# Kernel optimization log

Measured on AMD Instinct MI355X. Metric: run time of the kernel, lower is better.

## Reference

```python
import jax, jax.numpy as jnp
import numpy as np

N_QUBITS = 10
QLCU_LAYERS = 2
GATE_LAYERS = 2
FEATURE_DIM = 256
OUTPUT_DIM = 1
BATCH = 2048
TWO_PI = float(2.0 * np.pi)
N_MEAS = 3 * N_QUBITS


def _ang(theta, B):
    # broadcast scalar or (B,) angle to (B,) float32
    return jnp.broadcast_to(jnp.asarray(theta, jnp.float32), (B,))


def _apply_1q(psi, U, wire):
    # psi: (B,)+(2,)*n ; U: (B,2,2) complex64
    pm = jnp.moveaxis(psi, wire + 1, -1)
    out = jnp.einsum('bij,b...j->b...i', U, pm)
    return jnp.moveaxis(out, -1, wire + 1)


def rx(psi, theta, wire):
    B = psi.shape[0]
    t = _ang(theta, B) * 0.5
    c = jnp.cos(t).astype(jnp.complex64)
    s = (-1j) * jnp.sin(t).astype(jnp.complex64)
    U = jnp.stack([jnp.stack([c, s], -1), jnp.stack([s, c], -1)], -2)
    return _apply_1q(psi, U, wire)


def ry(psi, theta, wire):
    B = psi.shape[0]
    t = _ang(theta, B) * 0.5
    c = jnp.cos(t).astype(jnp.complex64)
    s = jnp.sin(t).astype(jnp.complex64)
    U = jnp.stack([jnp.stack([c, -s], -1), jnp.stack([s, c], -1)], -2)
    return _apply_1q(psi, U, wire)


def rz(psi, theta, wire):
    # diagonal: e^{-i t/2}, e^{+i t/2}
    B = psi.shape[0]
    n = psi.ndim - 1
    t = _ang(theta, B) * 0.5
    ph = jnp.exp(1j * jnp.stack([-t, t], -1).astype(jnp.complex64))  # (B,2)
    pm = jnp.moveaxis(psi, wire + 1, -1)
    pm = pm * ph.reshape((B,) + (1,) * (n - 1) + (2,))
    return jnp.moveaxis(pm, -1, wire + 1)


def _mv2(psi, a, b):
    return jnp.moveaxis(psi, (a + 1, b + 1), (-2, -1))


def _mv2_back(pm, a, b):
    return jnp.moveaxis(pm, (-2, -1), (a + 1, b + 1))


def crz(psi, theta, control, target):
    # diagonal on (control,target): [1, 1, e^{-it/2}, e^{+it/2}]
    B = psi.shape[0]
    n = psi.ndim - 1
    t = (_ang(theta, B) * 0.5).astype(jnp.complex64)
    e_m = jnp.exp(-1j * t)
    e_p = jnp.exp(1j * t)
    one = jnp.ones_like(e_m)
    P = jnp.stack([jnp.stack([one, one], -1), jnp.stack([e_m, e_p], -1)], -2)  # (B,2,2)
    pm = _mv2(psi, control, target)
    pm = pm * P.reshape((B,) + (1,) * (n - 2) + (2, 2))
    return _mv2_back(pm, control, target)


def ising_xx(psi, theta, a, b):
    # exp(-i t/2 XX): cos(t/2) I - i sin(t/2) X(x)X (bit-flip both)
    B = psi.shape[0]
    n = psi.ndim - 1
    t = _ang(theta, B) * 0.5
    c = jnp.cos(t).astype(jnp.complex64).reshape((B,) + (1,) * n)
    s = jnp.sin(t).astype(jnp.complex64).reshape((B,) + (1,) * n)
    pm = _mv2(psi, a, b)
    out = c * pm - 1j * s * pm[..., ::-1, ::-1]
    return _mv2_back(out, a, b)


def ising_yy(psi, theta, a, b):
    # exp(-i t/2 YY): (YY psi)[ta,tb] = (-1 if ta==tb else +1) * psi[flip]
    B = psi.shape[0]
    n = psi.ndim - 1
    t = _ang(theta, B) * 0.5
    c = jnp.cos(t).astype(jnp.complex64).reshape((B,) + (1,) * n)
    s = jnp.sin(t).astype(jnp.complex64).reshape((B,) + (1,) * n)
    sign = jnp.array([[-1.0, 1.0], [1.0, -1.0]], jnp.complex64)
    pm = _mv2(psi, a, b)
    out = c * pm - 1j * s * sign * pm[..., ::-1, ::-1]
    return _mv2_back(out, a, b)


def measure_xyz(psi):
    # expvals [X0..X_{n-1}, Y0.., Z0..] -> (B, 3n) float32
    n = psi.ndim - 1
    xs, ys, zs = [], [], []
    for w in range(n):
        pm = jnp.moveaxis(psi, w + 1, -1)
        p0, p1 = pm[..., 0], pm[..., 1]
        axes = tuple(range(1, n))
        a = jnp.sum(jnp.conj(p0) * p1, axis=axes)
        xs.append(2.0 * jnp.real(a))
        ys.append(2.0 * jnp.imag(a))
        zs.append(jnp.sum(jnp.abs(p0) ** 2 - jnp.abs(p1) ** 2, axis=axes))
    return jnp.stack(xs + ys + zs, axis=1).astype(jnp.float32)


def selective_ssm(psi, qlcu, bpar, cpar, dtpar, n, layers):
    idx = 0
    for _ in range(layers):
        for i in range(n):
            psi = ry(psi, qlcu[:, idx], i); idx += 1
        for i in range(n):
            psi = ising_xx(psi, qlcu[:, idx], i, (i + 1) % n); idx += 1
        for i in range(n):
            psi = ry(psi, bpar[i], i)
        for i in range(n):
            psi = ry(psi, qlcu[:, idx], i); idx += 1
        for i in range(n):
            psi = ising_yy(psi, qlcu[:, idx], i, (i + 1) % n); idx += 1
        for i in range(n):
            psi = rz(psi, cpar[i], i)
        for i in range(n):
            psi = rx(psi, dtpar[i], i)
    return psi


def gating(psi, gp, n, layers):
    idx = 0
    for _ in range(layers):
        for i in range(n):
            psi = rx(psi, gp[idx], i); idx += 1
        for i in range(n - 1):
            psi = crz(psi, gp[idx], i, i + 1); idx += 1
        for i in range(n):
            psi = ry(psi, gp[idx], i); idx += 1
        if n > 1:
            psi = crz(psi, gp[idx], n - 1, 0); idx += 1
    return psi


def skip_circuit(psi, sp, n):
    idx = 0
    for i in range(n):
        psi = rx(psi, sp[idx], i); idx += 1
    for i in range(n):
        psi = ry(psi, sp[idx], i); idx += 1
    for i in range(n):
        psi = rz(psi, sp[idx], i); idx += 1
    return psi


def _forward(x, W_proj, b_proj, qlcu_base, gate_base, skip_base, b_params, c_params, dt_params,
             W1, b1, W2, b2, W3, b3, w1, w2, w3, W_out, b_out):
    B = x.shape[0]
    n = N_QUBITS
    proj = x @ W_proj.T + b_proj
    qlcu = jax.nn.sigmoid(proj) * TWO_PI + qlcu_base[None, :]
    psi0 = jnp.zeros((B, 2 ** n), jnp.complex64).at[:, 0].set(1.0).reshape((B,) + (2,) * n)
    m1 = measure_xyz(selective_ssm(psi0, qlcu, b_params, c_params, dt_params, n, QLCU_LAYERS))
    # branches 2/3 have batch-independent params and initial state -> compute once, broadcast
    psi1 = jnp.zeros((1, 2 ** n), jnp.complex64).at[:, 0].set(1.0).reshape((1,) + (2,) * n)
    m2 = jnp.broadcast_to(measure_xyz(gating(psi1, gate_base, n, GATE_LAYERS)), (B, N_MEAS))
    m3 = jnp.broadcast_to(measure_xyz(skip_circuit(psi1, skip_base, n)), (B, N_MEAS))
    y1 = m1 @ W1.T + b1
    y2 = m2 @ W2.T + b2
    y3 = m3 @ W3.T + b3
    comb = w1 * y1 + w2 * y2 + w3 * y3
    return comb @ W_out.T + b_out


def setup_inputs() -> dict:
    key = jax.random.key(0)
    ks = jax.random.split(key, 17)
    nq = N_QUBITS
    n_qlcu = 4 * nq * QLCU_LAYERS
    n_gate = 4 * nq * GATE_LAYERS
    n_skip = 3 * nq
    lim_p = 1.0 / np.sqrt(FEATURE_DIM)
    lim_m = 1.0 / np.sqrt(N_MEAS)
    return dict(
        x=jax.random.normal(ks[0], (BATCH, FEATURE_DIM), jnp.float32),
        W_proj=jax.random.uniform(ks[1], (n_qlcu, FEATURE_DIM), jnp.float32, -lim_p, lim_p),
        b_proj=jax.random.uniform(ks[2], (n_qlcu,), jnp.float32, -lim_p, lim_p),
        qlcu_base=jax.random.uniform(ks[3], (n_qlcu,), jnp.float32, 0.0, TWO_PI),
        gate_base=jax.random.uniform(ks[4], (n_gate,), jnp.float32, 0.0, TWO_PI),
        skip_base=jax.random.uniform(ks[5], (n_skip,), jnp.float32, 0.0, TWO_PI),
        b_params=jax.random.uniform(ks[6], (nq,), jnp.float32, 0.0, TWO_PI),
        c_params=jax.random.uniform(ks[7], (nq,), jnp.float32, 0.0, TWO_PI),
        dt_params=jax.random.uniform(ks[8], (nq,), jnp.float32, 0.0, TWO_PI),
        W1=jax.random.uniform(ks[9], (N_MEAS, N_MEAS), jnp.float32, -lim_m, lim_m),
        b1=jax.random.uniform(ks[10], (N_MEAS,), jnp.float32, -lim_m, lim_m),
        W2=jax.random.uniform(ks[11], (N_MEAS, N_MEAS), jnp.float32, -lim_m, lim_m),
        b2=jax.random.uniform(ks[12], (N_MEAS,), jnp.float32, -lim_m, lim_m),
        W3=jax.random.uniform(ks[13], (N_MEAS, N_MEAS), jnp.float32, -lim_m, lim_m),
        b3=jax.random.uniform(ks[14], (N_MEAS,), jnp.float32, -lim_m, lim_m),
        w1=jnp.ones((1,), jnp.float32),
        w2=jnp.ones((1,), jnp.float32),
        w3=jnp.ones((1,), jnp.float32),
        W_out=jax.random.uniform(ks[15], (OUTPUT_DIM, N_MEAS), jnp.float32, -lim_m, lim_m),
        b_out=jax.random.uniform(ks[16], (OUTPUT_DIM,), jnp.float32, -lim_m, lim_m),
    )


def reference(x, W_proj, b_proj, qlcu_base, gate_base, skip_base, b_params, c_params, dt_params,
              W1, b1, W2, b2, W3, b3, w1, w2, w3, W_out, b_out):
    return _forward(x, W_proj, b_proj, qlcu_base, gate_base, skip_base, b_params, c_params, dt_params,
                    W1, b1, W2, b2, W3, b3, w1, w2, w3, W_out, b_out)
```

## Files before the change

### kernel.cpp

```cpp
#include <hip/hip_runtime.h>
#include <math.h>

#define TPB 320
#define TWO_PI_F 6.283185307179586f


#define ALLQ(OP) OP(0) OP(1) OP(2) OP(3) OP(4) OP(5) OP(6) OP(7) OP(8) OP(9)
#define ALLQ9(OP) OP(0) OP(1) OP(2) OP(3) OP(4) OP(5) OP(6) OP(7) OP(8)

template<int CTRL>
__device__ __forceinline__ float dppmv(float v) {
    return __builtin_bit_cast(float,
        __builtin_amdgcn_update_dpp(0, __builtin_bit_cast(int, v), CTRL, 0xF, 0xF, true));
}

template<int LM>
__device__ __forceinline__ float lx(float v, int lane) {
    (void)lane;
    if constexpr (LM == 1)       return dppmv<0xB1>(v);
    else if constexpr (LM == 2)  return dppmv<0x4E>(v);
    else if constexpr (LM == 3)  return dppmv<0x1B>(v);
    else if constexpr (LM == 4)  return dppmv<0x1B>(dppmv<0x141>(v));
    else if constexpr (LM == 6)  return dppmv<0xB1>(dppmv<0x141>(v));
    else if constexpr (LM == 8)  return dppmv<0x128>(v);
    else if constexpr (LM == 12) return dppmv<0x1B>(dppmv<0x140>(v));
    else                         return __shfl_xor(v, LM);
}


template<int W>
__device__ __forceinline__ void g_ry(float (&re)[16], float (&im)[16], float c, float s, int lane) {
    if constexpr (W <= 5) {
        constexpr int LM = 1 << (5 - W);
        const float ss = ((lane >> (5 - W)) & 1) ? s : -s;
        float pr[16], pi[16];
#pragma unroll
        for (int r = 0; r < 16; ++r) { pr[r] = lx<LM>(re[r], lane); pi[r] = lx<LM>(im[r], lane); }
#pragma unroll
        for (int r = 0; r < 16; ++r) {
            re[r] = fmaf(ss, pr[r], c * re[r]);
            im[r] = fmaf(ss, pi[r], c * im[r]);
        }
    } else {
        constexpr int MK = 1 << (9 - W);
#pragma unroll
        for (int r = 0; r < 16; ++r) {
            if ((r & MK) == 0) {
                const int r1 = r | MK;
                float r0 = re[r], i0 = im[r], r1v = re[r1], i1 = im[r1];
                re[r]  = fmaf(-s, r1v, c * r0);
                im[r]  = fmaf(-s, i1,  c * i0);
                re[r1] = fmaf( s, r0,  c * r1v);
                im[r1] = fmaf( s, i0,  c * i1);
            }
        }
    }
}

template<int W>
__device__ __forceinline__ void g_rx(float (&re)[16], float (&im)[16], float c, float s, int lane) {
    if constexpr (W <= 5) {
        constexpr int LM = 1 << (5 - W);
        float pr[16], pi[16];
#pragma unroll
        for (int r = 0; r < 16; ++r) { pr[r] = lx<LM>(re[r], lane); pi[r] = lx<LM>(im[r], lane); }
#pragma unroll
        for (int r = 0; r < 16; ++r) {
            re[r] = fmaf( s, pi[r], c * re[r]);
            im[r] = fmaf(-s, pr[r], c * im[r]);
        }
    } else {
        constexpr int MK = 1 << (9 - W);
#pragma unroll
        for (int r = 0; r < 16; ++r) {
            if ((r & MK) == 0) {
                const int r1 = r | MK;
                float r0 = re[r], i0 = im[r], r1v = re[r1], i1 = im[r1];
                re[r]  = fmaf( s, i1,  c * r0);
                im[r]  = fmaf(-s, r1v, c * i0);
                re[r1] = fmaf( s, i0,  c * r1v);
                im[r1] = fmaf(-s, r0,  c * i1);
            }
        }
    }
}

template<int W>
__device__ __forceinline__ void g_rz(float (&re)[16], float (&im)[16], float c, float s, int lane) {
    if constexpr (W <= 5) {
        const float sp = ((lane >> (5 - W)) & 1) ? s : -s;
#pragma unroll
        for (int r = 0; r < 16; ++r) {
            float rr = re[r], ii = im[r];
            re[r] = rr * c - ii * sp;
            im[r] = ii * c + rr * sp;
        }
    } else {
        constexpr int MK = 1 << (9 - W);
#pragma unroll
        for (int r = 0; r < 16; ++r) {
            const float sp = (r & MK) ? s : -s;
            float rr = re[r], ii = im[r];
            re[r] = rr * c - ii * sp;
            im[r] = ii * c + rr * sp;
        }
    }
}

template<int C, int T>
__device__ __forceinline__ void g_crz(float (&re)[16], float (&im)[16], float c, float s, int lane) {
#pragma unroll
    for (int r = 0; r < 16; ++r) {
        const int cb = (C <= 5) ? ((lane >> (5 - C)) & 1) : ((r >> (9 - C)) & 1);
        const int tb = (T <= 5) ? ((lane >> (5 - T)) & 1) : ((r >> (9 - T)) & 1);
        const float cc  = cb ? c : 1.f;
        const float sp2 = cb ? (tb ? s : -s) : 0.f;
        float rr = re[r], ii = im[r];
        re[r] = cc * rr - sp2 * ii;
        im[r] = cc * ii + sp2 * rr;
    }
}

template<int A, int Bq, bool YY>
__device__ __forceinline__ void g_xy(float (&re)[16], float (&im)[16], float c, float s, int lane) {
    constexpr int bpA = 9 - A, bpB = 9 - Bq;
    constexpr int LM   = ((bpA >= 4) ? (1 << (bpA - 4)) : 0) | ((bpB >= 4) ? (1 << (bpB - 4)) : 0);
    constexpr int LOCM = ((bpA < 4) ? (1 << bpA) : 0) | ((bpB < 4) ? (1 << bpB) : 0);
    float pr[16], pi[16];
#pragma unroll
    for (int r = 0; r < 16; ++r) {
        float vr = re[r ^ LOCM], vi = im[r ^ LOCM];
        if constexpr (LM != 0) { pr[r] = lx<LM>(vr, lane); pi[r] = lx<LM>(vi, lane); }
        else                   { pr[r] = vr; pi[r] = vi; }
    }
#pragma unroll
    for (int r = 0; r < 16; ++r) {
        float sg;
        if constexpr (YY) {
            const int bA = (A  <= 5) ? ((lane >> (5 - A )) & 1) : ((r >> (9 - A )) & 1);
            const int bB = (Bq <= 5) ? ((lane >> (5 - Bq)) & 1) : ((r >> (9 - Bq)) & 1);
            sg = (bA == bB) ? -s : s;
        } else sg = s;
        float rr = re[r], ii = im[r];
        re[r] = fmaf( sg, pi[r], c * rr);
        im[r] = fmaf(-sg, pr[r], c * ii);
    }
}

template<int W>
__device__ __forceinline__ void g_u1(float (&re)[16], float (&im)[16], const float* U, int lane) {
    const float u00r=U[0], u00i=U[1], u01r=U[2], u01i=U[3];
    const float u10r=U[4], u10i=U[5], u11r=U[6], u11i=U[7];
    if constexpr (W <= 5) {
        constexpr int LM = 1 << (5 - W);
        const int side = (lane >> (5 - W)) & 1;
        const float aR = side ? u11r : u00r, aI = side ? u11i : u00i;
        const float bR = side ? u10r : u01r, bI = side ? u10i : u01i;
        float pr[16], pi[16];
#pragma unroll
        for (int r = 0; r < 16; ++r) { pr[r] = lx<LM>(re[r], lane); pi[r] = lx<LM>(im[r], lane); }
#pragma unroll
        for (int r = 0; r < 16; ++r) {
            float rr = re[r], ii = im[r];
            float nr = aR * rr; nr = fmaf(-aI, ii, nr); nr = fmaf(bR, pr[r], nr); nr = fmaf(-bI, pi[r], nr);
            float ni = aR * ii; ni = fmaf( aI, rr, ni); ni = fmaf(bR, pi[r], ni); ni = fmaf( bI, pr[r], ni);
            re[r] = nr; im[r] = ni;
        }
    } else {
        constexpr int MK = 1 << (9 - W);
#pragma unroll
        for (int r = 0; r < 16; ++r) {
            if ((r & MK) == 0) {
                const int r1 = r | MK;
                float r0 = re[r], i0 = im[r], r1v = re[r1], i1 = im[r1];
                float a = u00r*r0; a = fmaf(-u00i, i0, a); a = fmaf(u01r, r1v, a); a = fmaf(-u01i, i1, a);
                float b = u00r*i0; b = fmaf( u00i, r0, b); b = fmaf(u01r, i1,  b); b = fmaf( u01i, r1v, b);
                float c = u10r*r0; c = fmaf(-u10i, i0, c); c = fmaf(u11r, r1v, c); c = fmaf(-u11i, i1, c);
                float d = u10r*i0; d = fmaf( u10i, r0, d); d = fmaf(u11r, i1,  d); d = fmaf( u11i, r1v, d);
                re[r] = a; im[r] = b; re[r1] = c; im[r1] = d;
            }
        }
    }
}


__device__ __forceinline__ void g_ry2_01(float (&re)[16], float (&im)[16],
                                         float c0, float s0, float c1, float s1, int lane) {
    float ar[16], ai[16], br[16], bi[16], cr2[16], ci2[16];
#pragma unroll
    for (int r = 0; r < 16; ++r) { ar[r] = lx<32>(re[r], lane); ai[r] = lx<32>(im[r], lane); }
#pragma unroll
    for (int r = 0; r < 16; ++r) { br[r] = lx<16>(re[r], lane); bi[r] = lx<16>(im[r], lane); }
#pragma unroll
    for (int r = 0; r < 16; ++r) { cr2[r] = lx<48>(re[r], lane); ci2[r] = lx<48>(im[r], lane); }
    const float sg0 = ((lane >> 5) & 1) ? s0 : -s0;
    const float sg1 = ((lane >> 4) & 1) ? s1 : -s1;
    const float k0 = c0 * c1, k1 = c1 * sg0, k2 = c0 * sg1, k3 = sg0 * sg1;
#pragma unroll
    for (int r = 0; r < 16; ++r) {
        float o_r = k0 * re[r];
        o_r = fmaf(k1, ar[r], o_r); o_r = fmaf(k2, br[r], o_r); o_r = fmaf(k3, cr2[r], o_r);
        float o_i = k0 * im[r];
        o_i = fmaf(k1, ai[r], o_i); o_i = fmaf(k2, bi[r], o_i); o_i = fmaf(k3, ci2[r], o_i);
        re[r] = o_r; im[r] = o_i;
    }
}

__device__ __forceinline__ void g_rx2_01(float (&re)[16], float (&im)[16],
                                         float c0, float s0, float c1, float s1, int lane) {
    float ar[16], ai[16], br[16], bi[16], cr2[16], ci2[16];
#pragma unroll
    for (int r = 0; r < 16; ++r) { ar[r] = lx<32>(re[r], lane); ai[r] = lx<32>(im[r], lane); }
#pragma unroll
    for (int r = 0; r < 16; ++r) { br[r] = lx<16>(re[r], lane); bi[r] = lx<16>(im[r], lane); }
#pragma unroll
    for (int r = 0; r < 16; ++r) { cr2[r] = lx<48>(re[r], lane); ci2[r] = lx<48>(im[r], lane); }
    const float k0 = c0 * c1, kA = c1 * s0, kB = c0 * s1, kC = s0 * s1;
#pragma unroll
    for (int r = 0; r < 16; ++r) {
        float rr = re[r], ii = im[r];
        float o_r = k0 * rr;
        o_r = fmaf(kA, ai[r], o_r); o_r = fmaf(kB, bi[r], o_r); o_r = fmaf(-kC, cr2[r], o_r);
        float o_i = k0 * ii;
        o_i = fmaf(-kA, ar[r], o_i); o_i = fmaf(-kB, br[r], o_i); o_i = fmaf(-kC, ci2[r], o_i);
        re[r] = o_r; im[r] = o_i;
    }
}

__device__ __forceinline__ void g_u2_01(float (&re)[16], float (&im)[16],
                                        const float* U0, const float* U1, int lane) {
    const int b0 = (lane >> 5) & 1, b1 = (lane >> 4) & 1;
    const float u0o_r = U0[(b0*2+b0)*2],       u0o_i = U0[(b0*2+b0)*2+1];
    const float u0f_r = U0[(b0*2+(b0^1))*2],   u0f_i = U0[(b0*2+(b0^1))*2+1];
    const float u1o_r = U1[(b1*2+b1)*2],       u1o_i = U1[(b1*2+b1)*2+1];
    const float u1f_r = U1[(b1*2+(b1^1))*2],   u1f_i = U1[(b1*2+(b1^1))*2+1];
    const float K00r = u0o_r*u1o_r - u0o_i*u1o_i, K00i = u0o_r*u1o_i + u0o_i*u1o_r;
    const float K01r = u0o_r*u1f_r - u0o_i*u1f_i, K01i = u0o_r*u1f_i + u0o_i*u1f_r;
    const float K10r = u0f_r*u1o_r - u0f_i*u1o_i, K10i = u0f_r*u1o_i + u0f_i*u1o_r;
    const float K11r = u0f_r*u1f_r - u0f_i*u1f_i, K11i = u0f_r*u1f_i + u0f_i*u1f_r;
    float ar[16], ai[16], br[16], bi[16], cr2[16], ci2[16];
#pragma unroll
    for (int r = 0; r < 16; ++r) { ar[r] = lx<32>(re[r], lane); ai[r] = lx<32>(im[r], lane); }
#pragma unroll
    for (int r = 0; r < 16; ++r) { br[r] = lx<16>(re[r], lane); bi[r] = lx<16>(im[r], lane); }
#pragma unroll
    for (int r = 0; r < 16; ++r) { cr2[r] = lx<48>(re[r], lane); ci2[r] = lx<48>(im[r], lane); }
#pragma unroll
    for (int r = 0; r < 16; ++r) {
        float rr = re[r], ii = im[r];
        float o_r = K00r * rr;         o_r = fmaf(-K00i, ii, o_r);
        o_r = fmaf(K01r, br[r], o_r);  o_r = fmaf(-K01i, bi[r], o_r);
        o_r = fmaf(K10r, ar[r], o_r);  o_r = fmaf(-K10i, ai[r], o_r);
        o_r = fmaf(K11r, cr2[r], o_r); o_r = fmaf(-K11i, ci2[r], o_r);
        float o_i = K00r * ii;         o_i = fmaf(K00i, rr, o_i);
        o_i = fmaf(K01r, bi[r], o_i);  o_i = fmaf(K01i, br[r], o_i);
        o_i = fmaf(K10r, ai[r], o_i);  o_i = fmaf(K10i, ar[r], o_i);
        o_i = fmaf(K11r, ci2[r], o_i); o_i = fmaf(K11i, cr2[r], o_i);
        re[r] = o_r; im[r] = o_i;
    }
}

__device__ __forceinline__ void g_ring2(float (&re)[16], float (&im)[16],
                                        float ca, float sa, float cb, float sb,
                                        bool yy, int lane) {
    float ar[16], ai[16], br[16], bi[16], cr2[16], ci2[16];
#pragma unroll
    for (int r = 0; r < 16; ++r) { ar[r] = lx<24>(re[r], lane); ai[r] = lx<24>(im[r], lane); }
#pragma unroll
    for (int r = 0; r < 16; ++r) { br[r] = lx<32>(re[r ^ 1], lane); bi[r] = lx<32>(im[r ^ 1], lane); }
#pragma unroll
    for (int r = 0; r < 16; ++r) { cr2[r] = lx<56>(re[r ^ 1], lane); ci2[r] = lx<56>(im[r ^ 1], lane); }
    float ka, kb0, kb1, kab0, kab1;
    if (yy) {
        const bool ea = (((lane >> 4) & 1) == ((lane >> 3) & 1));
        const float sga = ea ? -sa : sa;
        const int b0l = (lane >> 5) & 1;
        const float sgb0 = (0 == b0l) ? -sb : sb;
        const float sgb1 = (1 == b0l) ? -sb : sb;
        ka = cb * sga; kb0 = ca * sgb0; kb1 = ca * sgb1;
        kab0 = sga * sgb0; kab1 = sga * sgb1;
    } else {
        ka = cb * sa; kb0 = kb1 = ca * sb; kab0 = kab1 = sa * sb;
    }
    const float k0 = ca * cb;
#pragma unroll
    for (int r = 0; r < 16; ++r) {
        const float kb  = (r & 1) ? kb1  : kb0;
        const float kab = (r & 1) ? kab1 : kab0;
        float rr = re[r], ii = im[r];
        float o_r = k0 * rr;
        o_r = fmaf(ka, ai[r], o_r); o_r = fmaf(kb, bi[r], o_r); o_r = fmaf(-kab, cr2[r], o_r);
        float o_i = k0 * ii;
        o_i = fmaf(-ka, ar[r], o_i); o_i = fmaf(-kb, br[r], o_i); o_i = fmaf(-kab, ci2[r], o_i);
        re[r] = o_r; im[r] = o_i;
    }
}

__device__ __forceinline__ float wred(float v, int lane) {
    v += lx<1>(v, lane); v += lx<2>(v, lane); v += lx<4>(v, lane);
    v += lx<8>(v, lane); v += lx<16>(v, lane); v += lx<32>(v, lane);
    return v;
}

__device__ float meas_fold(const float (&re)[16], const float (&im)[16],
                           const float* __restrict__ V, int lane) {
    float oacc = 0.f;
    float q0r[16], q0i[16], q1r[16], q1i[16];
#pragma unroll
    for (int r = 0; r < 16; ++r) { q0r[r] = lx<32>(re[r], lane); q0i[r] = lx<32>(im[r], lane); }
#pragma unroll
    for (int r = 0; r < 16; ++r) { q1r[r] = lx<16>(re[r], lane); q1i[r] = lx<16>(im[r], lane); }

    float n2[16], n2s = 0.f;
#pragma unroll
    for (int r = 0; r < 16; ++r) { n2[r] = fmaf(re[r], re[r], im[r] * im[r]); n2s += n2[r]; }

#define M_LANE(w, LM_) { \
        float pr[16], pi[16]; \
        _Pragma("unroll") \
        for (int r = 0; r < 16; ++r) { pr[r] = lx<LM_>(re[r], lane); pi[r] = lx<LM_>(im[r], lane); } \
        float xa = 0.f, ya = 0.f; \
        _Pragma("unroll") \
        for (int r = 0; r < 16; ++r) { \
            xa = fmaf(re[r], pr[r], xa); xa = fmaf(im[r], pi[r], xa); \
            ya = fmaf(re[r], pi[r], ya); ya = fmaf(-im[r], pr[r], ya); \
        } \
        const float sg = ((lane >> (5 - w)) & 1) ? -1.f : 1.f; \
        oacc = fmaf(xa, V[w], oacc); \
        oacc = fmaf(sg * ya, V[10 + w], oacc); \
        oacc = fmaf(sg * n2s, V[20 + w], oacc); }
    M_LANE(2, 8) M_LANE(3, 4) M_LANE(4, 2) M_LANE(5, 1)
#undef M_LANE

#define M_REG(w, MK) { \
        float xa = 0.f, ya = 0.f, za = 0.f; \
        _Pragma("unroll") \
        for (int r = 0; r < 16; ++r) { \
            if ((r & MK) == 0) { \
                const int r1 = r | MK; \
                xa = fmaf(re[r], re[r1], xa); xa = fmaf(im[r], im[r1], xa); \
                ya = fmaf(re[r], im[r1], ya); ya = fmaf(-im[r], re[r1], ya); \
                za += n2[r] - n2[r1]; \
            } } \
        oacc = fmaf(2.f * xa, V[w], oacc); \
        oacc = fmaf(2.f * ya, V[10 + w], oacc); \
        oacc = fmaf(za, V[20 + w], oacc); }
    M_REG(6, 8) M_REG(7, 4) M_REG(8, 2) M_REG(9, 1)
#undef M_REG

    {
        float xa = 0.f, ya = 0.f;
#pragma unroll
        for (int r = 0; r < 16; ++r) {
            xa = fmaf(re[r], q0r[r], xa); xa = fmaf(im[r], q0i[r], xa);
            ya = fmaf(re[r], q0i[r], ya); ya = fmaf(-im[r], q0r[r], ya);
        }
        const float sg = ((lane >> 5) & 1) ? -1.f : 1.f;
        oacc = fmaf(xa, V[0], oacc);
        oacc = fmaf(sg * ya, V[10], oacc);
        oacc = fmaf(sg * n2s, V[20], oacc);
    }
    {
        float xa = 0.f, ya = 0.f;
#pragma unroll
        for (int r = 0; r < 16; ++r) {
            xa = fmaf(re[r], q1r[r], xa); xa = fmaf(im[r], q1i[r], xa);
            ya = fmaf(re[r], q1i[r], ya); ya = fmaf(-im[r], q1r[r], ya);
        }
        const float sg = ((lane >> 4) & 1) ? -1.f : 1.f;
        oacc = fmaf(xa, V[1], oacc);
        oacc = fmaf(sg * ya, V[11], oacc);
        oacc = fmaf(sg * n2s, V[21], oacc);
    }
    return oacc;
}

__device__ __forceinline__ void init_state(float (&re)[16], float (&im)[16], int lane) {
#pragma unroll
    for (int r = 0; r < 16; ++r) { re[r] = 0.f; im[r] = 0.f; }
    if (lane == 0) re[0] = 1.f;
}

__device__ void branch_gating(const float* __restrict__ gb,
                              const float* __restrict__ b1,
                              const float* __restrict__ W2, const float* __restrict__ b2,
                              const float* __restrict__ w1p, const float* __restrict__ w2p,
                              const float* __restrict__ Wout, const float* __restrict__ bout,
                              float* __restrict__ vbr, float* __restrict__ ws_c, int lane) {
    const float w1v = w1p[0], w2v = w2p[0];
    float bias = 0.f;
    if (lane < 30) {
        float v = 0.f;
        for (int k = 0; k < 30; ++k) v = fmaf(Wout[k], W2[k * 30 + lane], v);
        vbr[lane] = w2v * v;
        bias = Wout[lane] * (w1v * b1[lane] + w2v * b2[lane]);
    }

    float re[16], im[16];
    init_state(re, im, lane);
    for (int L = 0; L < 2; ++L) {
        const int g0 = L * 30;
        {
            float c0_, s0_, c1_, s1_;
            __sincosf(0.5f * gb[g0 + 0], &s0_, &c0_);
            __sincosf(0.5f * gb[g0 + 1], &s1_, &c1_);
            g_rx2_01(re, im, c0_, s0_, c1_, s1_, lane);
        }
#define BRX(i) { float s_, c_; __sincosf(0.5f * gb[g0 + i], &s_, &c_); g_rx<i>(re, im, c_, s_, lane); }
        BRX(2) BRX(3) BRX(4) BRX(5) BRX(6) BRX(7) BRX(8) BRX(9)
#undef BRX
#define BCRZ(i) { float s_, c_; __sincosf(0.5f * gb[g0 + 10 + i], &s_, &c_); g_crz<i, i + 1>(re, im, c_, s_, lane); }
        ALLQ9(BCRZ)
#undef BCRZ
        {
            float c0_, s0_, c1_, s1_;
            __sincosf(0.5f * gb[g0 + 19 + 0], &s0_, &c0_);
            __sincosf(0.5f * gb[g0 + 19 + 1], &s1_, &c1_);
            g_ry2_01(re, im, c0_, s0_, c1_, s1_, lane);
        }
#define BRY(i) { float s_, c_; __sincosf(0.5f * gb[g0 + 19 + i], &s_, &c_); g_ry<i>(re, im, c_, s_, lane); }
        BRY(2) BRY(3) BRY(4) BRY(5) BRY(6) BRY(7) BRY(8) BRY(9)
#undef BRY
        { float s_, c_; __sincosf(0.5f * gb[g0 + 29], &s_, &c_); g_crz<9, 0>(re, im, c_, s_, lane); }
    }

    float oacc = meas_fold(re, im, vbr, lane) + bias;
    oacc = wred(oacc, lane);
    if (lane == 0) ws_c[0] = oacc + bout[0];
}

__device__ void branch_skip(const float* __restrict__ sp,
                            const float* __restrict__ W3, const float* __restrict__ b3v,
                            const float* __restrict__ w3p,
                            const float* __restrict__ Wout,
                            float* __restrict__ ws_c, int lane) {
    float vk = 0.f;
    if (lane < 30) {
        const int q = (lane < 10) ? lane : ((lane < 20) ? lane - 10 : lane - 20);
        float c1, s1, c2, s2, c3, s3;
        __sincosf(0.5f * sp[q],      &s1, &c1);
        __sincosf(0.5f * sp[10 + q], &s2, &c2);
        __sincosf(0.5f * sp[20 + q], &s3, &c3);
        float a2r = c2 * c1, a2i = s2 * s1, b2r = s2 * c1, b2i = -c2 * s1;
        float a3r = fmaf(a2i,  s3, a2r * c3), a3i = fmaf(-a2r, s3, a2i * c3);
        float b3r = fmaf(-b2i, s3, b2r * c3), b3i = fmaf( b2r, s3, b2i * c3);
        float m;
        if (lane < 10)      m = 2.f * (a3r * b3r + a3i * b3i);
        else if (lane < 20) m = 2.f * (a3r * b3i - a3i * b3r);
        else                m = (a3r * a3r + a3i * a3i) - (b3r * b3r + b3i * b3i);
        float v = 0.f;
        for (int k = 0; k < 30; ++k) v = fmaf(Wout[k], W3[k * 30 + lane], v);
        vk = w3p[0] * fmaf(m, v, Wout[lane] * b3v[lane]);
    }
    vk = wred(vk, lane);
    if (lane == 0) ws_c[0] = vk;
}


__global__ void __launch_bounds__(TPB) k_main(
    const float* __restrict__ x, const float* __restrict__ Wp,
    const float* __restrict__ bp_, const float* __restrict__ qb,
    const float* __restrict__ bpar, const float* __restrict__ cpar, const float* __restrict__ dtpar,
    const float* __restrict__ gb, const float* __restrict__ sp,
    const float* __restrict__ W1, const float* __restrict__ b1,
    const float* __restrict__ W2, const float* __restrict__ b2,
    const float* __restrict__ W3, const float* __restrict__ b3,
    const float* __restrict__ w1p, const float* __restrict__ w2p, const float* __restrict__ w3p,
    const float* __restrict__ Wout, const float* __restrict__ bout,
    float* __restrict__ ws, int B) {

    const int wv = threadIdx.x >> 6, lane = threadIdx.x & 63;

    __shared__ float vbr[32];

    if (wv == 4) {
        if (blockIdx.x == 0) {
            branch_gating(gb, b1, W2, b2, w1p, w2p, Wout, bout, vbr, ws + B, lane);
            if (gridDim.x == 1) branch_skip(sp, W3, b3, w3p, Wout, ws + B + 1, lane);
        } else if (blockIdx.x == 1) {
            branch_skip(sp, W3, b3, w3p, Wout, ws + B + 1, lane);
        }
        return;
    }

    const int b = blockIdx.x * 4 + wv;
    const int bb = (b < B) ? b : (B - 1);

    __shared__ float proj[4][80];
    __shared__ float ac1[4][10], as1[4][10], ac2[4][10], as2[4][10];
    __shared__ float gc[4][60], gs[4][60];
    __shared__ float ub[4][80];
    __shared__ float uraw[4][32], uu[4][32];

    const int sub = lane & 15, grp = lane >> 4;
    float4 xv[4];
    {
        const float* xr = x + (size_t)bb * 256 + sub * 16;
#pragma unroll
        for (int j = 0; j < 4; ++j) xv[j] = reinterpret_cast<const float4*>(xr)[j];
    }
#pragma unroll 4
    for (int p = 0; p < 20; ++p) {
        const int row = p * 4 + grp;
        const float* wr = Wp + (size_t)row * 256 + sub * 16;
        float acc = 0.f;
#pragma unroll
        for (int j = 0; j < 4; ++j) {
            float4 w4 = reinterpret_cast<const float4*>(wr)[j];
            acc = fmaf(xv[j].x, w4.x, acc); acc = fmaf(xv[j].y, w4.y, acc);
            acc = fmaf(xv[j].z, w4.z, acc); acc = fmaf(xv[j].w, w4.w, acc);
        }
        acc += lx<1>(acc, lane); acc += lx<2>(acc, lane);
        acc += lx<4>(acc, lane); acc += lx<8>(acc, lane);
        if (sub == 0) proj[wv][row] = acc;
    }

    {
#define DO_ANGLE(IDX) { \
        const int idx = (IDX); \
        float ang = TWO_PI_F / (1.f + __expf(-(proj[wv][idx] + bp_[idx]))) + qb[idx]; \
        const int l = (idx >= 40) ? 1 : 0; \
        const int p = idx - 40 * l; \
        float s_, c_; \
        if (p < 10) { \
            __sincosf(0.5f * ang, &s_, &c_); \
            if (l == 0) { ac1[wv][p] = c_; as1[wv][p] = s_; } \
            else        { ac2[wv][p] = c_; as2[wv][p] = s_; } \
        } else if (p < 20) { \
            __sincosf(0.5f * ang, &s_, &c_); \
            gc[wv][l * 30 + p - 10] = c_; gs[wv][l * 30 + p - 10] = s_; \
        } else if (p < 30) { \
            __sincosf(0.5f * (ang + bpar[p - 20]), &s_, &c_); \
            gc[wv][l * 30 + 10 + p - 20] = c_; gs[wv][l * 30 + 10 + p - 20] = s_; \
        } else { \
            __sincosf(0.5f * ang, &s_, &c_); \
            gc[wv][l * 30 + 20 + p - 30] = c_; gs[wv][l * 30 + 20 + p - 30] = s_; \
        } }
        DO_ANGLE(lane)
        if (lane < 16) DO_ANGLE(64 + lane)
#undef DO_ANGLE

        if (lane < 30) {
            float ut = 0.f;
            for (int k = 0; k < 30; ++k) ut = fmaf(Wout[k], W1[k * 30 + lane], ut);
            uraw[wv][lane] = w1p[0] * ut;
        }
        if (lane < 10) {
            float ca = ac2[wv][lane], sa = as2[wv][lane];
            float cg2, sg2, cd2, sd2;
            __sincosf(0.5f * cpar[lane],  &sg2, &cg2);
            __sincosf(0.5f * dtpar[lane], &sd2, &cd2);
            float A = ca * cd2, Bv = sa * sd2;
            float C = -sa * cd2, D = -ca * sd2;
            float E = sa * cd2,  F = -ca * sd2;
            float G = ca * cd2,  H = -sa * sd2;
            float* U = &ub[wv][lane * 8];
            U[0] = cg2 * A + sg2 * Bv;  U[1] = cg2 * Bv - sg2 * A;
            U[2] = cg2 * C - sg2 * D;   U[3] = sg2 * C + cg2 * D;
            U[4] = cg2 * E + sg2 * F;   U[5] = cg2 * F - sg2 * E;
            U[6] = cg2 * G - sg2 * H;   U[7] = sg2 * G + cg2 * H;

            float cg, sgf, cd, sdf;
            __sincosf(cpar[lane],  &sgf, &cg);
            __sincosf(dtpar[lane], &sdf, &cd);
            float uX = uraw[wv][lane], uY = uraw[wv][10 + lane], uZ = uraw[wv][20 + lane];
            uu[wv][lane]      =  uX * cg + uY * cd * sgf + uZ * sdf * sgf;
            uu[wv][10 + lane] = -uX * sgf + uY * cd * cg + uZ * sdf * cg;
            uu[wv][20 + lane] = -uY * sdf + uZ * cd;
        }
    }

    float re[16], im[16];
    {
        const float* AC = ac1[wv]; const float* AS = as1[wv];
        float pl = ((lane >> 5) & 1) ? AS[0] : AC[0];
        pl *= ((lane >> 4) & 1) ? AS[1] : AC[1];
        pl *= ((lane >> 3) & 1) ? AS[2] : AC[2];
        pl *= ((lane >> 2) & 1) ? AS[3] : AC[3];
        pl *= ((lane >> 1) & 1) ? AS[4] : AC[4];
        pl *= ( lane       & 1) ? AS[5] : AC[5];
#pragma unroll
        for (int r = 0; r < 16; ++r) {
            float p = ((r >> 3) & 1) ? AS[6] : AC[6];
            p *= ((r >> 2) & 1) ? AS[7] : AC[7];
            p *= ((r >> 1) & 1) ? AS[8] : AC[8];
            p *= ( r       & 1) ? AS[9] : AC[9];
            re[r] = pl * p; im[r] = 0.f;
        }
    }

    const float* GC = gc[wv]; const float* GS = gs[wv];

#define RING(base, YYf) \
    g_ring2(re, im, GC[(base)+1], GS[(base)+1], GC[(base)+9], GS[(base)+9], YYf, lane); \
    g_xy<2, 3, YYf>(re, im, GC[(base)+2], GS[(base)+2], lane); \
    g_xy<3, 4, YYf>(re, im, GC[(base)+3], GS[(base)+3], lane); \
    g_xy<4, 5, YYf>(re, im, GC[(base)+4], GS[(base)+4], lane); \
    g_xy<5, 6, YYf>(re, im, GC[(base)+5], GS[(base)+5], lane); \
    g_xy<6, 7, YYf>(re, im, GC[(base)+6], GS[(base)+6], lane); \
    g_xy<7, 8, YYf>(re, im, GC[(base)+7], GS[(base)+7], lane); \
    g_xy<8, 9, YYf>(re, im, GC[(base)+8], GS[(base)+8], lane); \
    g_xy<0, 1, YYf>(re, im, GC[(base)+0], GS[(base)+0], lane);

    RING(0, false)
    g_ry2_01(re, im, GC[10], GS[10], GC[11], GS[11], lane);
#define G_CD1(i) g_ry<i>(re, im, GC[10 + i], GS[10 + i], lane);
    G_CD1(2) G_CD1(3) G_CD1(4) G_CD1(5) G_CD1(6) G_CD1(7) G_CD1(8) G_CD1(9)
#undef G_CD1
    RING(20, true)
    g_u2_01(re, im, &ub[wv][0], &ub[wv][8], lane);
#define G_UB(i) g_u1<i>(re, im, &ub[wv][i * 8], lane);
    G_UB(2) G_UB(3) G_UB(4) G_UB(5) G_UB(6) G_UB(7) G_UB(8) G_UB(9)
#undef G_UB
    RING(30, false)
    g_ry2_01(re, im, GC[40], GS[40], GC[41], GS[41], lane);
#define G_CD2(i) g_ry<i>(re, im, GC[40 + i], GS[40 + i], lane);
    G_CD2(2) G_CD2(3) G_CD2(4) G_CD2(5) G_CD2(6) G_CD2(7) G_CD2(8) G_CD2(9)
#undef G_CD2
    RING(50, true)
#undef RING

    float oacc = meas_fold(re, im, uu[wv], lane);
    oacc = wred(oacc, lane);
    if (lane == 0 && b < B) ws[b] = oacc;
}

__global__ void k_out(const float* __restrict__ ws, float* __restrict__ out, int B) {
    int i = blockIdx.x * blockDim.x + threadIdx.x;
    if (i < B) out[i] = ws[i] + ws[B] + ws[B + 1];
}

extern "C" void kernel_launch(void* const* d_in, const int* in_sizes, int n_in,
                              void* d_out, int out_size, void* d_ws, size_t ws_size,
                              hipStream_t stream) {
    const float* x         = (const float*)d_in[0];
    const float* W_proj    = (const float*)d_in[1];
    const float* b_proj    = (const float*)d_in[2];
    const float* qlcu_base = (const float*)d_in[3];
    const float* gate_base = (const float*)d_in[4];
    const float* skip_base = (const float*)d_in[5];
    const float* b_params  = (const float*)d_in[6];
    const float* c_params  = (const float*)d_in[7];
    const float* dt_params = (const float*)d_in[8];
    const float* W1    = (const float*)d_in[9];
    const float* b1    = (const float*)d_in[10];
    const float* W2    = (const float*)d_in[11];
    const float* b2    = (const float*)d_in[12];
    const float* W3    = (const float*)d_in[13];
    const float* b3    = (const float*)d_in[14];
    const float* w1    = (const float*)d_in[15];
    const float* w2    = (const float*)d_in[16];
    const float* w3    = (const float*)d_in[17];
    const float* W_out = (const float*)d_in[18];
    const float* b_out = (const float*)d_in[19];
    float* out = (float*)d_out;
    float* ws  = (float*)d_ws;

    const int B = in_sizes[0] / 256;
    const int nb = (B + 3) / 4;

    hipLaunchKernelGGL(k_main, dim3(nb), dim3(TPB), 0, stream,
                       x, W_proj, b_proj, qlcu_base, b_params, c_params, dt_params,
                       gate_base, skip_base, W1, b1, W2, b2, W3, b3, w1, w2, w3,
                       W_out, b_out, ws, B);
    hipLaunchKernelGGL(k_out, dim3((B + 255) / 256), dim3(256), 0, stream, ws, out, B);
}
```

Measured before the change: 48.59 us.

## Process two batch samples per wavefront with interleaved dual-state gate kernels

Each wavefront now simulates two independent 10-qubit state vectors at once, with dual versions of the RY, XX/YY, single-qubit unitary and measurement routines that interleave the two states' cross-lane exchanges and arithmetic. This is meant to hide DPP/shuffle latency and amortise the per-sample parameter setup. It drops the earlier specialised fused two-gate paths (ring2, u2_01, ry2_01) in favour of uniform per-gate dual calls. Blocks shrink to 256 threads covering 8 samples, and register pressure roughly doubles, which risks lower occupancy or spills.

Measured after the change: 56.09 us. +15.4%, slower.

```diff
diff --git a/kernel.cpp b/kernel.cpp
--- a/kernel.cpp
+++ b/kernel.cpp
@@ -1,7 +1,7 @@
 #include <hip/hip_runtime.h>
 #include <math.h>
 
-#define TPB 320
+#define TPB 256
 #define TWO_PI_F 6.283185307179586f
 
 
@@ -27,6 +27,12 @@
     else                         return __shfl_xor(v, LM);
 }
 
+template<int W>
+__device__ __forceinline__ int qbit(int lane, int r) {
+    if constexpr (W <= 5) return (lane >> (5 - W)) & 1;
+    else                  return (r >> (9 - W)) & 1;
+}
+
 
 template<int W>
 __device__ __forceinline__ void g_ry(float (&re)[16], float (&im)[16], float c, float s, int lane) {
@@ -85,34 +91,12 @@
     }
 }
 
-template<int W>
-__device__ __forceinline__ void g_rz(float (&re)[16], float (&im)[16], float c, float s, int lane) {
-    if constexpr (W <= 5) {
-        const float sp = ((lane >> (5 - W)) & 1) ? s : -s;
-#pragma unroll
-        for (int r = 0; r < 16; ++r) {
-            float rr = re[r], ii = im[r];
-            re[r] = rr * c - ii * sp;
-            im[r] = ii * c + rr * sp;
-        }
-    } else {
-        constexpr int MK = 1 << (9 - W);
-#pragma unroll
-        for (int r = 0; r < 16; ++r) {
-            const float sp = (r & MK) ? s : -s;
-            float rr = re[r], ii = im[r];
-            re[r] = rr * c - ii * sp;
-            im[r] = ii * c + rr * sp;
-        }
-    }
-}
-
 template<int C, int T>
 __device__ __forceinline__ void g_crz(float (&re)[16], float (&im)[16], float c, float s, int lane) {
 #pragma unroll
     for (int r = 0; r < 16; ++r) {
-        const int cb = (C <= 5) ? ((lane >> (5 - C)) & 1) : ((r >> (9 - C)) & 1);
-        const int tb = (T <= 5) ? ((lane >> (5 - T)) & 1) : ((r >> (9 - T)) & 1);
+        const int cb = qbit<C>(lane, r);
+        const int tb = qbit<T>(lane, r);
         const float cc  = cb ? c : 1.f;
         const float sp2 = cb ? (tb ? s : -s) : 0.f;
         float rr = re[r], ii = im[r];
@@ -120,69 +104,6 @@
         im[r] = cc * ii + sp2 * rr;
     }
 }
-
-template<int A, int Bq, bool YY>
-__device__ __forceinline__ void g_xy(float (&re)[16], float (&im)[16], float c, float s, int lane) {
-    constexpr int bpA = 9 - A, bpB = 9 - Bq;
-    constexpr int LM   = ((bpA >= 4) ? (1 << (bpA - 4)) : 0) | ((bpB >= 4) ? (1 << (bpB - 4)) : 0);
-    constexpr int LOCM = ((bpA < 4) ? (1 << bpA) : 0) | ((bpB < 4) ? (1 << bpB) : 0);
-    float pr[16], pi[16];
-#pragma unroll
-    for (int r = 0; r < 16; ++r) {
-        float vr = re[r ^ LOCM], vi = im[r ^ LOCM];
-        if constexpr (LM != 0) { pr[r] = lx<LM>(vr, lane); pi[r] = lx<LM>(vi, lane); }
-        else                   { pr[r] = vr; pi[r] = vi; }
-    }
-#pragma unroll
-    for (int r = 0; r < 16; ++r) {
-        float sg;
-        if constexpr (YY) {
-            const int bA = (A  <= 5) ? ((lane >> (5 - A )) & 1) : ((r >> (9 - A )) & 1);
-            const int bB = (Bq <= 5) ? ((lane >> (5 - Bq)) & 1) : ((r >> (9 - Bq)) & 1);
-            sg = (bA == bB) ? -s : s;
-        } else sg = s;
-        float rr = re[r], ii = im[r];
-        re[r] = fmaf( sg, pi[r], c * rr);
-        im[r] = fmaf(-sg, pr[r], c * ii);
-    }
-}
-
-template<int W>
-__device__ __forceinline__ void g_u1(float (&re)[16], float (&im)[16], const float* U, int lane) {
-    const float u00r=U[0], u00i=U[1], u01r=U[2], u01i=U[3];
-    const float u10r=U[4], u10i=U[5], u11r=U[6], u11i=U[7];
-    if constexpr (W <= 5) {
-        constexpr int LM = 1 << (5 - W);
-        const int side = (lane >> (5 - W)) & 1;
-        const float aR = side ? u11r : u00r, aI = side ? u11i : u00i;
-        const float bR = side ? u10r : u01r, bI = side ? u10i : u01i;
-        float pr[16], pi[16];
-#pragma unroll
-        for (int r = 0; r < 16; ++r) { pr[r] = lx<LM>(re[r], lane); pi[r] = lx<LM>(im[r], lane); }
-#pragma unroll
-        for (int r = 0; r < 16; ++r) {
-            float rr = re[r], ii = im[r];
-            float nr = aR * rr; nr = fmaf(-aI, ii, nr); nr = fmaf(bR, pr[r], nr); nr = fmaf(-bI, pi[r], nr);
-            float ni = aR * ii; ni = fmaf( aI, rr, ni); ni = fmaf(bR, pi[r], ni); ni = fmaf( bI, pr[r], ni);
-            re[r] = nr; im[r] = ni;
-        }
-    } else {
-        constexpr int MK = 1 << (9 - W);
-#pragma unroll
-        for (int r = 0; r < 16; ++r) {
-            if ((r & MK) == 0) {
-                const int r1 = r | MK;
-                float r0 = re[r], i0 = im[r], r1v = re[r1], i1 = im[r1];
-                float a = u00r*r0; a = fmaf(-u00i, i0, a); a = fmaf(u01r, r1v, a); a = fmaf(-u01i, i1, a);
-                float b = u00r*i0; b = fmaf( u00i, r0, b); b = fmaf(u01r, i1,  b); b = fmaf( u01i, r1v, b);
-                float c = u10r*r0; c = fmaf(-u10i, i0, c); c = fmaf(u11r, r1v, c); c = fmaf(-u11i, i1, c);
-                float d = u10r*i0; d = fmaf( u10i, r0, d); d = fmaf(u11r, i1,  d); d = fmaf( u11i, r1v, d);
-                re[r] = a; im[r] = b; re[r1] = c; im[r1] = d;
-            }
-        }
-    }
-}
-
 
 __device__ __forceinline__ void g_ry2_01(float (&re)[16], float (&im)[16],
                                          float c0, float s0, float c1, float s1, int lane) {
@@ -227,75 +148,6 @@
     }
 }
 
-__device__ __forceinline__ void g_u2_01(float (&re)[16], float (&im)[16],
-                                        const float* U0, const float* U1, int lane) {
-    const int b0 = (lane >> 5) & 1, b1 = (lane >> 4) & 1;
-    const float u0o_r = U0[(b0*2+b0)*2],       u0o_i = U0[(b0*2+b0)*2+1];
-    const float u0f_r = U0[(b0*2+(b0^1))*2],   u0f_i = U0[(b0*2+(b0^1))*2+1];
-    const float u1o_r = U1[(b1*2+b1)*2],       u1o_i = U1[(b1*2+b1)*2+1];
-    const float u1f_r = U1[(b1*2+(b1^1))*2],   u1f_i = U1[(b1*2+(b1^1))*2+1];
-    const float K00r = u0o_r*u1o_r - u0o_i*u1o_i, K00i = u0o_r*u1o_i + u0o_i*u1o_r;
-    const float K01r = u0o_r*u1f_r - u0o_i*u1f_i, K01i = u0o_r*u1f_i + u0o_i*u1f_r;
-    const float K10r = u0f_r*u1o_r - u0f_i*u1o_i, K10i = u0f_r*u1o_i + u0f_i*u1o_r;
-    const float K11r = u0f_r*u1f_r - u0f_i*u1f_i, K11i = u0f_r*u1f_i + u0f_i*u1f_r;
-    float ar[16], ai[16], br[16], bi[16], cr2[16], ci2[16];
-#pragma unroll
-    for (int r = 0; r < 16; ++r) { ar[r] = lx<32>(re[r], lane); ai[r] = lx<32>(im[r], lane); }
-#pragma unroll
-    for (int r = 0; r < 16; ++r) { br[r] = lx<16>(re[r], lane); bi[r] = lx<16>(im[r], lane); }
-#pragma unroll
-    for (int r = 0; r < 16; ++r) { cr2[r] = lx<48>(re[r], lane); ci2[r] = lx<48>(im[r], lane); }
-#pragma unroll
-    for (int r = 0; r < 16; ++r) {
-        float rr = re[r], ii = im[r];
-        float o_r = K00r * rr;         o_r = fmaf(-K00i, ii, o_r);
-        o_r = fmaf(K01r, br[r], o_r);  o_r = fmaf(-K01i, bi[r], o_r);
-        o_r = fmaf(K10r, ar[r], o_r);  o_r = fmaf(-K10i, ai[r], o_r);
-        o_r = fmaf(K11r, cr2[r], o_r); o_r = fmaf(-K11i, ci2[r], o_r);
-        float o_i = K00r * ii;         o_i = fmaf(K00i, rr, o_i);
-        o_i = fmaf(K01r, bi[r], o_i);  o_i = fmaf(K01i, br[r], o_i);
-        o_i = fmaf(K10r, ai[r], o_i);  o_i = fmaf(K10i, ar[r], o_i);
-        o_i = fmaf(K11r, ci2[r], o_i); o_i = fmaf(K11i, cr2[r], o_i);
-        re[r] = o_r; im[r] = o_i;
-    }
-}
-
-__device__ __forceinline__ void g_ring2(float (&re)[16], float (&im)[16],
-                                        float ca, float sa, float cb, float sb,
-                                        bool yy, int lane) {
-    float ar[16], ai[16], br[16], bi[16], cr2[16], ci2[16];
-#pragma unroll
-    for (int r = 0; r < 16; ++r) { ar[r] = lx<24>(re[r], lane); ai[r] = lx<24>(im[r], lane); }
-#pragma unroll
-    for (int r = 0; r < 16; ++r) { br[r] = lx<32>(re[r ^ 1], lane); bi[r] = lx<32>(im[r ^ 1], lane); }
-#pragma unroll
-    for (int r = 0; r < 16; ++r) { cr2[r] = lx<56>(re[r ^ 1], lane); ci2[r] = lx<56>(im[r ^ 1], lane); }
-    float ka, kb0, kb1, kab0, kab1;
-    if (yy) {
-        const bool ea = (((lane >> 4) & 1) == ((lane >> 3) & 1));
-        const float sga = ea ? -sa : sa;
-        const int b0l = (lane >> 5) & 1;
-        const float sgb0 = (0 == b0l) ? -sb : sb;
-        const float sgb1 = (1 == b0l) ? -sb : sb;
-        ka = cb * sga; kb0 = ca * sgb0; kb1 = ca * sgb1;
-        kab0 = sga * sgb0; kab1 = sga * sgb1;
-    } else {
-        ka = cb * sa; kb0 = kb1 = ca * sb; kab0 = kab1 = sa * sb;
-    }
-    const float k0 = ca * cb;
-#pragma unroll
-    for (int r = 0; r < 16; ++r) {
-        const float kb  = (r & 1) ? kb1  : kb0;
-        const float kab = (r & 1) ? kab1 : kab0;
-        float rr = re[r], ii = im[r];
-        float o_r = k0 * rr;
-        o_r = fmaf(ka, ai[r], o_r); o_r = fmaf(kb, bi[r], o_r); o_r = fmaf(-kab, cr2[r], o_r);
-        float o_i = k0 * ii;
-        o_i = fmaf(-ka, ar[r], o_i); o_i = fmaf(-kb, br[r], o_i); o_i = fmaf(-kab, ci2[r], o_i);
-        re[r] = o_r; im[r] = o_i;
-    }
-}
-
 __device__ __forceinline__ float wred(float v, int lane) {
     v += lx<1>(v, lane); v += lx<2>(v, lane); v += lx<4>(v, lane);
     v += lx<8>(v, lane); v += lx<16>(v, lane); v += lx<32>(v, lane);
@@ -305,12 +157,6 @@
 __device__ float meas_fold(const float (&re)[16], const float (&im)[16],
                            const float* __restrict__ V, int lane) {
     float oacc = 0.f;
-    float q0r[16], q0i[16], q1r[16], q1i[16];
-#pragma unroll
-    for (int r = 0; r < 16; ++r) { q0r[r] = lx<32>(re[r], lane); q0i[r] = lx<32>(im[r], lane); }
-#pragma unroll
-    for (int r = 0; r < 16; ++r) { q1r[r] = lx<16>(re[r], lane); q1i[r] = lx<16>(im[r], lane); }
-
     float n2[16], n2s = 0.f;
 #pragma unroll
     for (int r = 0; r < 16; ++r) { n2[r] = fmaf(re[r], re[r], im[r] * im[r]); n2s += n2[r]; }
@@ -329,7 +175,7 @@
         oacc = fmaf(xa, V[w], oacc); \
         oacc = fmaf(sg * ya, V[10 + w], oacc); \
         oacc = fmaf(sg * n2s, V[20 + w], oacc); }
-    M_LANE(2, 8) M_LANE(3, 4) M_LANE(4, 2) M_LANE(5, 1)
+    M_LANE(0, 32) M_LANE(1, 16) M_LANE(2, 8) M_LANE(3, 4) M_LANE(4, 2) M_LANE(5, 1)
 #undef M_LANE
 
 #define M_REG(w, MK) { \
@@ -347,39 +193,215 @@
         oacc = fmaf(za, V[20 + w], oacc); }
     M_REG(6, 8) M_REG(7, 4) M_REG(8, 2) M_REG(9, 1)
 #undef M_REG
-
-    {
-        float xa = 0.f, ya = 0.f;
-#pragma unroll
-        for (int r = 0; r < 16; ++r) {
-            xa = fmaf(re[r], q0r[r], xa); xa = fmaf(im[r], q0i[r], xa);
-            ya = fmaf(re[r], q0i[r], ya); ya = fmaf(-im[r], q0r[r], ya);
-        }
-        const float sg = ((lane >> 5) & 1) ? -1.f : 1.f;
-        oacc = fmaf(xa, V[0], oacc);
-        oacc = fmaf(sg * ya, V[10], oacc);
-        oacc = fmaf(sg * n2s, V[20], oacc);
-    }
-    {
-        float xa = 0.f, ya = 0.f;
-#pragma unroll
-        for (int r = 0; r < 16; ++r) {
-            xa = fmaf(re[r], q1r[r], xa); xa = fmaf(im[r], q1i[r], xa);
-            ya = fmaf(re[r], q1i[r], ya); ya = fmaf(-im[r], q1r[r], ya);
-        }
-        const float sg = ((lane >> 4) & 1) ? -1.f : 1.f;
-        oacc = fmaf(xa, V[1], oacc);
-        oacc = fmaf(sg * ya, V[11], oacc);
-        oacc = fmaf(sg * n2s, V[21], oacc);
-    }
     return oacc;
 }
 
-__device__ __forceinline__ void init_state(float (&re)[16], float (&im)[16], int lane) {
+__device__ __forceinline__ void init_zero(float (&re)[16], float (&im)[16], int lane) {
 #pragma unroll
     for (int r = 0; r < 16; ++r) { re[r] = 0.f; im[r] = 0.f; }
     if (lane == 0) re[0] = 1.f;
 }
+
+
+template<int W>
+__device__ __forceinline__ void g_ry_d(float (&re0)[16], float (&im0)[16],
+                                       float (&re1)[16], float (&im1)[16],
+                                       float cA, float sA, float cB, float sB, int lane) {
+    if constexpr (W <= 5) {
+        constexpr int LM = 1 << (5 - W);
+        const int bit = (lane >> (5 - W)) & 1;
+        const float ssA = bit ? sA : -sA;
+        const float ssB = bit ? sB : -sB;
+        float p0r[16], p0i[16], p1r[16], p1i[16];
+#pragma unroll
+        for (int r = 0; r < 16; ++r) { p0r[r] = lx<LM>(re0[r], lane); p0i[r] = lx<LM>(im0[r], lane); }
+#pragma unroll
+        for (int r = 0; r < 16; ++r) { p1r[r] = lx<LM>(re1[r], lane); p1i[r] = lx<LM>(im1[r], lane); }
+#pragma unroll
+        for (int r = 0; r < 16; ++r) {
+            re0[r] = fmaf(ssA, p0r[r], cA * re0[r]);
+            im0[r] = fmaf(ssA, p0i[r], cA * im0[r]);
+        }
+#pragma unroll
+        for (int r = 0; r < 16; ++r) {
+            re1[r] = fmaf(ssB, p1r[r], cB * re1[r]);
+            im1[r] = fmaf(ssB, p1i[r], cB * im1[r]);
+        }
+    } else {
+        constexpr int MK = 1 << (9 - W);
+#pragma unroll
+        for (int r = 0; r < 16; ++r) {
+            if ((r & MK) == 0) {
+                const int r1 = r | MK;
+                float a = re0[r], b = im0[r], c2 = re0[r1], d = im0[r1];
+                re0[r]  = fmaf(-sA, c2, cA * a);
+                im0[r]  = fmaf(-sA, d,  cA * b);
+                re0[r1] = fmaf( sA, a,  cA * c2);
+                im0[r1] = fmaf( sA, b,  cA * d);
+                float e = re1[r], f = im1[r], g = re1[r1], h = im1[r1];
+                re1[r]  = fmaf(-sB, g, cB * e);
+                im1[r]  = fmaf(-sB, h, cB * f);
+                re1[r1] = fmaf( sB, e, cB * g);
+                im1[r1] = fmaf( sB, f, cB * h);
+            }
+        }
+    }
+}
+
+template<int A, int Bq, bool YY>
+__device__ __forceinline__ void g_xy_d(float (&re0)[16], float (&im0)[16],
+                                       float (&re1)[16], float (&im1)[16],
+                                       float cA, float sA, float cB, float sB, int lane) {
+    constexpr int bpA = 9 - A, bpB = 9 - Bq;
+    constexpr int LM   = ((bpA >= 4) ? (1 << (bpA - 4)) : 0) | ((bpB >= 4) ? (1 << (bpB - 4)) : 0);
+    constexpr int LOCM = ((bpA < 4) ? (1 << bpA) : 0) | ((bpB < 4) ? (1 << bpB) : 0);
+    float p0r[16], p0i[16], p1r[16], p1i[16];
+#pragma unroll
+    for (int r = 0; r < 16; ++r) {
+        float vr = re0[r ^ LOCM], vi = im0[r ^ LOCM];
+        if constexpr (LM != 0) { p0r[r] = lx<LM>(vr, lane); p0i[r] = lx<LM>(vi, lane); }
+        else                   { p0r[r] = vr; p0i[r] = vi; }
+    }
+#pragma unroll
+    for (int r = 0; r < 16; ++r) {
+        float vr = re1[r ^ LOCM], vi = im1[r ^ LOCM];
+        if constexpr (LM != 0) { p1r[r] = lx<LM>(vr, lane); p1i[r] = lx<LM>(vi, lane); }
+        else                   { p1r[r] = vr; p1i[r] = vi; }
+    }
+#pragma unroll
+    for (int r = 0; r < 16; ++r) {
+        float sgA, sgB;
+        if constexpr (YY) {
+            const int bA = qbit<A>(lane, r);
+            const int bB = qbit<Bq>(lane, r);
+            sgA = (bA == bB) ? -sA : sA;
+            sgB = (bA == bB) ? -sB : sB;
+        } else { sgA = sA; sgB = sB; }
+        {
+            float rr = re0[r], ii = im0[r];
+            re0[r] = fmaf( sgA, p0i[r], cA * rr);
+            im0[r] = fmaf(-sgA, p0r[r], cA * ii);
+        }
+        {
+            float rr = re1[r], ii = im1[r];
+            re1[r] = fmaf( sgB, p1i[r], cB * rr);
+            im1[r] = fmaf(-sgB, p1r[r], cB * ii);
+        }
+    }
+}
+
+template<int W>
+__device__ __forceinline__ void g_u1_d(float (&re0)[16], float (&im0)[16],
+                                       float (&re1)[16], float (&im1)[16],
+                                       const float* U0, const float* U1, int lane) {
+    if constexpr (W <= 5) {
+        constexpr int LM = 1 << (5 - W);
+        const int side = (lane >> (5 - W)) & 1;
+        const float aR0 = side ? U0[6] : U0[0], aI0 = side ? U0[7] : U0[1];
+        const float bR0 = side ? U0[4] : U0[2], bI0 = side ? U0[5] : U0[3];
+        const float aR1 = side ? U1[6] : U1[0], aI1 = side ? U1[7] : U1[1];
+        const float bR1 = side ? U1[4] : U1[2], bI1 = side ? U1[5] : U1[3];
+        float p0r[16], p0i[16], p1r[16], p1i[16];
+#pragma unroll
+        for (int r = 0; r < 16; ++r) { p0r[r] = lx<LM>(re0[r], lane); p0i[r] = lx<LM>(im0[r], lane); }
+#pragma unroll
+        for (int r = 0; r < 16; ++r) { p1r[r] = lx<LM>(re1[r], lane); p1i[r] = lx<LM>(im1[r], lane); }
+#pragma unroll
+        for (int r = 0; r < 16; ++r) {
+            float rr = re0[r], ii = im0[r];
+            float nr = aR0 * rr; nr = fmaf(-aI0, ii, nr); nr = fmaf(bR0, p0r[r], nr); nr = fmaf(-bI0, p0i[r], nr);
+            float ni = aR0 * ii; ni = fmaf( aI0, rr, ni); ni = fmaf(bR0, p0i[r], ni); ni = fmaf( bI0, p0r[r], ni);
+            re0[r] = nr; im0[r] = ni;
+        }
+#pragma unroll
+        for (int r = 0; r < 16; ++r) {
+            float rr = re1[r], ii = im1[r];
+            float nr = aR1 * rr; nr = fmaf(-aI1, ii, nr); nr = fmaf(bR1, p1r[r], nr); nr = fmaf(-bI1, p1i[r], nr);
+            float ni = aR1 * ii; ni = fmaf( aI1, rr, ni); ni = fmaf(bR1, p1i[r], ni); ni = fmaf( bI1, p1r[r], ni);
+            re1[r] = nr; im1[r] = ni;
+        }
+    } else {
+        constexpr int MK = 1 << (9 - W);
+#pragma unroll
+        for (int r = 0; r < 16; ++r) {
+            if ((r & MK) == 0) {
+                const int r1 = r | MK;
+                {
+                    float r0 = re0[r], i0 = im0[r], r1v = re0[r1], i1 = im0[r1];
+                    float a = U0[0]*r0; a = fmaf(-U0[1], i0, a); a = fmaf(U0[2], r1v, a); a = fmaf(-U0[3], i1, a);
+                    float b = U0[0]*i0; b = fmaf( U0[1], r0, b); b = fmaf(U0[2], i1,  b); b = fmaf( U0[3], r1v, b);
+                    float c = U0[4]*r0; c = fmaf(-U0[5], i0, c); c = fmaf(U0[6], r1v, c); c = fmaf(-U0[7], i1, c);
+                    float d = U0[4]*i0; d = fmaf( U0[5], r0, d); d = fmaf(U0[6], i1,  d); d = fmaf( U0[7], r1v, d);
+                    re0[r] = a; im0[r] = b; re0[r1] = c; im0[r1] = d;
+                }
+                {
+                    float r0 = re1[r], i0 = im1[r], r1v = re1[r1], i1 = im1[r1];
+                    float a = U1[0]*r0; a = fmaf(-U1[1], i0, a); a = fmaf(U1[2], r1v, a); a = fmaf(-U1[3], i1, a);
+                    float b = U1[0]*i0; b = fmaf( U1[1], r0, b); b = fmaf(U1[2], i1,  b); b = fmaf( U1[3], r1v, b);
+                    float c = U1[4]*r0; c = fmaf(-U1[5], i0, c); c = fmaf(U1[6], r1v, c); c = fmaf(-U1[7], i1, c);
+                    float d = U1[4]*i0; d = fmaf( U1[5], r0, d); d = fmaf(U1[6], i1,  d); d = fmaf( U1[7], r1v, d);
+                    re1[r] = a; im1[r] = b; re1[r1] = c; im1[r1] = d;
+                }
+            }
+        }
+    }
+}
+
+__device__ void meas_fold_d(const float (&re0)[16], const float (&im0)[16],
+                            const float (&re1)[16], const float (&im1)[16],
+                            const float* __restrict__ V, int lane,
+                            float& o0out, float& o1out) {
+    float o0 = 0.f, o1 = 0.f;
+    float n2s0 = 0.f, n2s1 = 0.f;
+#pragma unroll
+    for (int r = 0; r < 16; ++r) { n2s0 = fmaf(re0[r], re0[r], n2s0); n2s0 = fmaf(im0[r], im0[r], n2s0); }
+#pragma unroll
+    for (int r = 0; r < 16; ++r) { n2s1 = fmaf(re1[r], re1[r], n2s1); n2s1 = fmaf(im1[r], im1[r], n2s1); }
+
+#define MD_LANE(w, LM_) { \
+        float p0r[16], p0i[16], p1r[16], p1i[16]; \
+        _Pragma("unroll") \
+        for (int r = 0; r < 16; ++r) { p0r[r] = lx<LM_>(re0[r], lane); p0i[r] = lx<LM_>(im0[r], lane); } \
+        _Pragma("unroll") \
+        for (int r = 0; r < 16; ++r) { p1r[r] = lx<LM_>(re1[r], lane); p1i[r] = lx<LM_>(im1[r], lane); } \
+        float xa0 = 0.f, ya0 = 0.f, xa1 = 0.f, ya1 = 0.f; \
+        _Pragma("unroll") \
+        for (int r = 0; r < 16; ++r) { \
+            xa0 = fmaf(re0[r], p0r[r], xa0); xa0 = fmaf(im0[r], p0i[r], xa0); \
+            ya0 = fmaf(re0[r], p0i[r], ya0); ya0 = fmaf(-im0[r], p0r[r], ya0); \
+        } \
+        _Pragma("unroll") \
+        for (int r = 0; r < 16; ++r) { \
+            xa1 = fmaf(re1[r], p1r[r], xa1); xa1 = fmaf(im1[r], p1i[r], xa1); \
+            ya1 = fmaf(re1[r], p1i[r], ya1); ya1 = fmaf(-im1[r], p1r[r], ya1); \
+        } \
+        const float sg = ((lane >> (5 - w)) & 1) ? -1.f : 1.f; \
+        o0 = fmaf(xa0, V[w], o0); o0 = fmaf(sg * ya0, V[10 + w], o0); o0 = fmaf(sg * n2s0, V[20 + w], o0); \
+        o1 = fmaf(xa1, V[w], o1); o1 = fmaf(sg * ya1, V[10 + w], o1); o1 = fmaf(sg * n2s1, V[20 + w], o1); }
+    MD_LANE(0, 32) MD_LANE(1, 16) MD_LANE(2, 8) MD_LANE(3, 4) MD_LANE(4, 2) MD_LANE(5, 1)
+#undef MD_LANE
+
+#define MD_REG(w, MK) { \
+        float xa0 = 0.f, ya0 = 0.f, za0 = 0.f, xa1 = 0.f, ya1 = 0.f, za1 = 0.f; \
+        _Pragma("unroll") \
+        for (int r = 0; r < 16; ++r) { \
+            if ((r & MK) == 0) { \
+                const int r1 = r | MK; \
+                xa0 = fmaf(re0[r], re0[r1], xa0); xa0 = fmaf(im0[r], im0[r1], xa0); \
+                ya0 = fmaf(re0[r], im0[r1], ya0); ya0 = fmaf(-im0[r], re0[r1], ya0); \
+                za0 += fmaf(re0[r], re0[r], im0[r] * im0[r]) - fmaf(re0[r1], re0[r1], im0[r1] * im0[r1]); \
+                xa1 = fmaf(re1[r], re1[r1], xa1); xa1 = fmaf(im1[r], im1[r1], xa1); \
+                ya1 = fmaf(re1[r], im1[r1], ya1); ya1 = fmaf(-im1[r], re1[r1], ya1); \
+                za1 += fmaf(re1[r], re1[r], im1[r] * im1[r]) - fmaf(re1[r1], re1[r1], im1[r1] * im1[r1]); \
+            } } \
+        o0 = fmaf(2.f * xa0, V[w], o0); o0 = fmaf(2.f * ya0, V[10 + w], o0); o0 = fmaf(za0, V[20 + w], o0); \
+        o1 = fmaf(2.f * xa1, V[w], o1); o1 = fmaf(2.f * ya1, V[10 + w], o1); o1 = fmaf(za1, V[20 + w], o1); }
+    MD_REG(6, 8) MD_REG(7, 4) MD_REG(8, 2) MD_REG(9, 1)
+#undef MD_REG
+
+    o0out = o0; o1out = o1;
+}
+
 
 __device__ void branch_gating(const float* __restrict__ gb,
                               const float* __restrict__ b1,
@@ -397,7 +419,7 @@
     }
 
     float re[16], im[16];
-    init_state(re, im, lane);
+    init_zero(re, im, lane);
     for (int L = 0; L < 2; ++L) {
         const int g0 = L * 30;
         {
@@ -457,7 +479,7 @@
 }
 
 
-__global__ void __launch_bounds__(TPB) k_main(
+__global__ void __launch_bounds__(TPB, 1) k_main(
     const float* __restrict__ x, const float* __restrict__ Wp,
     const float* __restrict__ bp_, const float* __restrict__ qb,
     const float* __restrict__ bpar, const float* __restrict__ cpar, const float* __restrict__ dtpar,
@@ -473,71 +495,77 @@
 
     __shared__ float vbr[32];
 
-    if (wv == 4) {
-        if (blockIdx.x == 0) {
-            branch_gating(gb, b1, W2, b2, w1p, w2p, Wout, bout, vbr, ws + B, lane);
-            if (gridDim.x == 1) branch_skip(sp, W3, b3, w3p, Wout, ws + B + 1, lane);
-        } else if (blockIdx.x == 1) {
-            branch_skip(sp, W3, b3, w3p, Wout, ws + B + 1, lane);
-        }
+    if (blockIdx.x == gridDim.x - 1) {
+        if (wv == 0) branch_gating(gb, b1, W2, b2, w1p, w2p, Wout, bout, vbr, ws + B, lane);
+        else if (wv == 1) branch_skip(sp, W3, b3, w3p, Wout, ws + B + 1, lane);
         return;
     }
 
-    const int b = blockIdx.x * 4 + wv;
-    const int bb = (b < B) ? b : (B - 1);
-
-    __shared__ float proj[4][80];
-    __shared__ float ac1[4][10], as1[4][10], ac2[4][10], as2[4][10];
-    __shared__ float gc[4][60], gs[4][60];
-    __shared__ float ub[4][80];
+    const int b0 = blockIdx.x * 8 + wv * 2;
+    const int b1i = b0 + 1;
+    const int bb0 = (b0 < B) ? b0 : (B - 1);
+    const int bb1 = (b1i < B) ? b1i : (B - 1);
+
+    __shared__ float proj[4][2][80];
+    __shared__ float ac1[4][2][10], as1[4][2][10], ac2[4][2][10], as2[4][2][10];
+    __shared__ float gc[4][2][60], gs[4][2][60];
+    __shared__ float ub[4][2][80];
     __shared__ float uraw[4][32], uu[4][32];
 
     const int sub = lane & 15, grp = lane >> 4;
-    float4 xv[4];
+    float4 xv0[4], xv1[4];
     {
-        const float* xr = x + (size_t)bb * 256 + sub * 16;
-#pragma unroll
-        for (int j = 0; j < 4; ++j) xv[j] = reinterpret_cast<const float4*>(xr)[j];
+        const float* xr0 = x + (size_t)bb0 * 256 + sub * 16;
+        const float* xr1 = x + (size_t)bb1 * 256 + sub * 16;
+#pragma unroll
+        for (int j = 0; j < 4; ++j) xv0[j] = reinterpret_cast<const float4*>(xr0)[j];
+#pragma unroll
+        for (int j = 0; j < 4; ++j) xv1[j] = reinterpret_cast<const float4*>(xr1)[j];
     }
 #pragma unroll 4
     for (int p = 0; p < 20; ++p) {
         const int row = p * 4 + grp;
         const float* wr = Wp + (size_t)row * 256 + sub * 16;
-        float acc = 0.f;
+        float a0 = 0.f, a1 = 0.f;
 #pragma unroll
         for (int j = 0; j < 4; ++j) {
             float4 w4 = reinterpret_cast<const float4*>(wr)[j];
-            acc = fmaf(xv[j].x, w4.x, acc); acc = fmaf(xv[j].y, w4.y, acc);
-            acc = fmaf(xv[j].z, w4.z, acc); acc = fmaf(xv[j].w, w4.w, acc);
-        }
-        acc += lx<1>(acc, lane); acc += lx<2>(acc, lane);
-        acc += lx<4>(acc, lane); acc += lx<8>(acc, lane);
-        if (sub == 0) proj[wv][row] = acc;
+            a0 = fmaf(xv0[j].x, w4.x, a0); a0 = fmaf(xv0[j].y, w4.y, a0);
+            a0 = fmaf(xv0[j].z, w4.z, a0); a0 = fmaf(xv0[j].w, w4.w, a0);
+            a1 = fmaf(xv1[j].x, w4.x, a1); a1 = fmaf(xv1[j].y, w4.y, a1);
+            a1 = fmaf(xv1[j].z, w4.z, a1); a1 = fmaf(xv1[j].w, w4.w, a1);
+        }
+        a0 += lx<1>(a0, lane); a1 += lx<1>(a1, lane);
+        a0 += lx<2>(a0, lane); a1 += lx<2>(a1, lane);
+        a0 += lx<4>(a0, lane); a1 += lx<4>(a1, lane);
+        a0 += lx<8>(a0, lane); a1 += lx<8>(a1, lane);
+        if (sub == 0) { proj[wv][0][row] = a0; proj[wv][1][row] = a1; }
     }
 
     {
-#define DO_ANGLE(IDX) { \
+#define DO_ANGLE(E, IDX) { \
         const int idx = (IDX); \
-        float ang = TWO_PI_F / (1.f + __expf(-(proj[wv][idx] + bp_[idx]))) + qb[idx]; \
+        float ang = TWO_PI_F / (1.f + __expf(-(proj[wv][E][idx] + bp_[idx]))) + qb[idx]; \
         const int l = (idx >= 40) ? 1 : 0; \
         const int p = idx - 40 * l; \
         float s_, c_; \
         if (p < 10) { \
             __sincosf(0.5f * ang, &s_, &c_); \
-            if (l == 0) { ac1[wv][p] = c_; as1[wv][p] = s_; } \
-            else        { ac2[wv][p] = c_; as2[wv][p] = s_; } \
+            if (l == 0) { ac1[wv][E][p] = c_; as1[wv][E][p] = s_; } \
+            else        { ac2[wv][E][p] = c_; as2[wv][E][p] = s_; } \
         } else if (p < 20) { \
             __sincosf(0.5f * ang, &s_, &c_); \
-            gc[wv][l * 30 + p - 10] = c_; gs[wv][l * 30 + p - 10] = s_; \
+            gc[wv][E][l * 30 + p - 10] = c_; gs[wv][E][l * 30 + p - 10] = s_; \
         } else if (p < 30) { \
             __sincosf(0.5f * (ang + bpar[p - 20]), &s_, &c_); \
-            gc[wv][l * 30 + 10 + p - 20] = c_; gs[wv][l * 30 + 10 + p - 20] = s_; \
+            gc[wv][E][l * 30 + 10 + p - 20] = c_; gs[wv][E][l * 30 + 10 + p - 20] = s_; \
         } else { \
             __sincosf(0.5f * ang, &s_, &c_); \
-            gc[wv][l * 30 + 20 + p - 30] = c_; gs[wv][l * 30 + 20 + p - 30] = s_; \
+            gc[wv][E][l * 30 + 20 + p - 30] = c_; gs[wv][E][l * 30 + 20 + p - 30] = s_; \
         } }
-        DO_ANGLE(lane)
-        if (lane < 16) DO_ANGLE(64 + lane)
+        DO_ANGLE(0, lane)
+        DO_ANGLE(1, lane)
+        if (lane < 16) { DO_ANGLE(0, 64 + lane) DO_ANGLE(1, 64 + lane) }
 #undef DO_ANGLE
 
         if (lane < 30) {
@@ -546,20 +574,6 @@
             uraw[wv][lane] = w1p[0] * ut;
         }
         if (lane < 10) {
-            float ca = ac2[wv][lane], sa = as2[wv][lane];
-            float cg2, sg2, cd2, sd2;
-            __sincosf(0.5f * cpar[lane],  &sg2, &cg2);
-            __sincosf(0.5f * dtpar[lane], &sd2, &cd2);
-            float A = ca * cd2, Bv = sa * sd2;
-            float C = -sa * cd2, D = -ca * sd2;
-            float E = sa * cd2,  F = -ca * sd2;
-            float G = ca * cd2,  H = -sa * sd2;
-            float* U = &ub[wv][lane * 8];
-            U[0] = cg2 * A + sg2 * Bv;  U[1] = cg2 * Bv - sg2 * A;
-            U[2] = cg2 * C - sg2 * D;   U[3] = sg2 * C + cg2 * D;
-            U[4] = cg2 * E + sg2 * F;   U[5] = cg2 * F - sg2 * E;
-            U[6] = cg2 * G - sg2 * H;   U[7] = sg2 * G + cg2 * H;
-
             float cg, sgf, cd, sdf;
             __sincosf(cpar[lane],  &sgf, &cg);
             __sincosf(dtpar[lane], &sdf, &cd);
@@ -568,11 +582,28 @@
             uu[wv][10 + lane] = -uX * sgf + uY * cd * cg + uZ * sdf * cg;
             uu[wv][20 + lane] = -uY * sdf + uZ * cd;
         }
-    }
-
-    float re[16], im[16];
+        const int eSel = (lane >= 32) ? 1 : 0;
+        const int ql = lane - 32 * eSel;
+        if (ql < 10) {
+            float ca = ac2[wv][eSel][ql], sa = as2[wv][eSel][ql];
+            float cg2, sg2, cd2, sd2;
+            __sincosf(0.5f * cpar[ql],  &sg2, &cg2);
+            __sincosf(0.5f * dtpar[ql], &sd2, &cd2);
+            float A = ca * cd2, Bv = sa * sd2;
+            float C = -sa * cd2, D = -ca * sd2;
+            float E = sa * cd2,  F = -ca * sd2;
+            float G = ca * cd2,  H = -sa * sd2;
+            float* U = &ub[wv][eSel][ql * 8];
+            U[0] = cg2 * A + sg2 * Bv;  U[1] = cg2 * Bv - sg2 * A;
+            U[2] = cg2 * C - sg2 * D;   U[3] = sg2 * C + cg2 * D;
+            U[4] = cg2 * E + sg2 * F;   U[5] = cg2 * F - sg2 * E;
+            U[6] = cg2 * G - sg2 * H;   U[7] = sg2 * G + cg2 * H;
+        }
+    }
+
+    float re0[16], im0[16], re1[16], im1[16];
     {
-        const float* AC = ac1[wv]; const float* AS = as1[wv];
+        const float* AC = ac1[wv][0]; const float* AS = as1[wv][0];
         float pl = ((lane >> 5) & 1) ? AS[0] : AC[0];
         pl *= ((lane >> 4) & 1) ? AS[1] : AC[1];
         pl *= ((lane >> 3) & 1) ? AS[2] : AC[2];
@@ -585,44 +616,74 @@
             p *= ((r >> 2) & 1) ? AS[7] : AC[7];
             p *= ((r >> 1) & 1) ? AS[8] : AC[8];
             p *= ( r       & 1) ? AS[9] : AC[9];
-            re[r] = pl * p; im[r] = 0.f;
-        }
-    }
-
-    const float* GC = gc[wv]; const float* GS = gs[wv];
-
-#define RING(base, YYf) \
-    g_ring2(re, im, GC[(base)+1], GS[(base)+1], GC[(base)+9], GS[(base)+9], YYf, lane); \
-    g_xy<2, 3, YYf>(re, im, GC[(base)+2], GS[(base)+2], lane); \
-    g_xy<3, 4, YYf>(re, im, GC[(base)+3], GS[(base)+3], lane); \
-    g_xy<4, 5, YYf>(re, im, GC[(base)+4], GS[(base)+4], lane); \
-    g_xy<5, 6, YYf>(re, im, GC[(base)+5], GS[(base)+5], lane); \
-    g_xy<6, 7, YYf>(re, im, GC[(base)+6], GS[(base)+6], lane); \
-    g_xy<7, 8, YYf>(re, im, GC[(base)+7], GS[(base)+7], lane); \
-    g_xy<8, 9, YYf>(re, im, GC[(base)+8], GS[(base)+8], lane); \
-    g_xy<0, 1, YYf>(re, im, GC[(base)+0], GS[(base)+0], lane);
-
-    RING(0, false)
-    g_ry2_01(re, im, GC[10], GS[10], GC[11], GS[11], lane);
-#define G_CD1(i) g_ry<i>(re, im, GC[10 + i], GS[10 + i], lane);
-    G_CD1(2) G_CD1(3) G_CD1(4) G_CD1(5) G_CD1(6) G_CD1(7) G_CD1(8) G_CD1(9)
-#undef G_CD1
-    RING(20, true)
-    g_u2_01(re, im, &ub[wv][0], &ub[wv][8], lane);
-#define G_UB(i) g_u1<i>(re, im, &ub[wv][i * 8], lane);
-    G_UB(2) G_UB(3) G_UB(4) G_UB(5) G_UB(6) G_UB(7) G_UB(8) G_UB(9)
-#undef G_UB
-    RING(30, false)
-    g_ry2_01(re, im, GC[40], GS[40], GC[41], GS[41], lane);
-#define G_CD2(i) g_ry<i>(re, im, GC[40 + i], GS[40 + i], lane);
-    G_CD2(2) G_CD2(3) G_CD2(4) G_CD2(5) G_CD2(6) G_CD2(7) G_CD2(8) G_CD2(9)
-#undef G_CD2
-    RING(50, true)
-#undef RING
-
-    float oacc = meas_fold(re, im, uu[wv], lane);
-    oacc = wred(oacc, lane);
-    if (lane == 0 && b < B) ws[b] = oacc;
+            re0[r] = pl * p; im0[r] = 0.f;
+        }
+    }
+    {
+        const float* AC = ac1[wv][1]; const float* AS = as1[wv][1];
+        float pl = ((lane >> 5) & 1) ? AS[0] : AC[0];
+        pl *= ((lane >> 4) & 1) ? AS[1] : AC[1];
+        pl *= ((lane >> 3) & 1) ? AS[2] : AC[2];
+        pl *= ((lane >> 2) & 1) ? AS[3] : AC[3];
+        pl *= ((lane >> 1) & 1) ? AS[4] : AC[4];
+        pl *= ( lane       & 1) ? AS[5] : AC[5];
+#pragma unroll
+        for (int r = 0; r < 16; ++r) {
+            float p = ((r >> 3) & 1) ? AS[6] : AC[6];
+            p *= ((r >> 2) & 1) ? AS[7] : AC[7];
+            p *= ((r >> 1) & 1) ? AS[8] : AC[8];
+            p *= ( r       & 1) ? AS[9] : AC[9];
+            re1[r] = pl * p; im1[r] = 0.f;
+        }
+    }
+
+    const float* GC0 = gc[wv][0]; const float* GS0 = gs[wv][0];
+    const float* GC1 = gc[wv][1]; const float* GS1 = gs[wv][1];
+
+#define RING_D(base, YYf) \
+    g_xy_d<0, 1, YYf>(re0, im0, re1, im1, GC0[(base)+0], GS0[(base)+0], GC1[(base)+0], GS1[(base)+0], lane); \
+    g_xy_d<1, 2, YYf>(re0, im0, re1, im1, GC0[(base)+1], GS0[(base)+1], GC1[(base)+1], GS1[(base)+1], lane); \
+    g_xy_d<2, 3, YYf>(re0, im0, re1, im1, GC0[(base)+2], GS0[(base)+2], GC1[(base)+2], GS1[(base)+2], lane); \
+    g_xy_d<3, 4, YYf>(re0, im0, re1, im1, GC0[(base)+3], GS0[(base)+3], GC1[(base)+3], GS1[(base)+3], lane); \
+    g_xy_d<4, 5, YYf>(re0, im0, re1, im1, GC0[(base)+4], GS0[(base)+4], GC1[(base)+4], GS1[(base)+4], lane); \
+    g_xy_d<5, 6, YYf>(re0, im0, re1, im1, GC0[(base)+5], GS0[(base)+5], GC1[(base)+5], GS1[(base)+5], lane); \
+    g_xy_d<6, 7, YYf>(re0, im0, re1, im1, GC0[(base)+6], GS0[(base)+6], GC1[(base)+6], GS1[(base)+6], lane); \
+    g_xy_d<7, 8, YYf>(re0, im0, re1, im1, GC0[(base)+7], GS0[(base)+7], GC1[(base)+7], GS1[(base)+7], lane); \
+    g_xy_d<8, 9, YYf>(re0, im0, re1, im1, GC0[(base)+8], GS0[(base)+8], GC1[(base)+8], GS1[(base)+8], lane); \
+    g_xy_d<9, 0, YYf>(re0, im0, re1, im1, GC0[(base)+9], GS0[(base)+9], GC1[(base)+9], GS1[(base)+9], lane);
+
+#define CD_D(base) \
+    g_ry_d<0>(re0, im0, re1, im1, GC0[(base)+0], GS0[(base)+0], GC1[(base)+0], GS1[(base)+0], lane); \
+    g_ry_d<1>(re0, im0, re1, im1, GC0[(base)+1], GS0[(base)+1], GC1[(base)+1], GS1[(base)+1], lane); \
+    g_ry_d<2>(re0, im0, re1, im1, GC0[(base)+2], GS0[(base)+2], GC1[(base)+2], GS1[(base)+2], lane); \
+    g_ry_d<3>(re0, im0, re1, im1, GC0[(base)+3], GS0[(base)+3], GC1[(base)+3], GS1[(base)+3], lane); \
+    g_ry_d<4>(re0, im0, re1, im1, GC0[(base)+4], GS0[(base)+4], GC1[(base)+4], GS1[(base)+4], lane); \
+    g_ry_d<5>(re0, im0, re1, im1, GC0[(base)+5], GS0[(base)+5], GC1[(base)+5], GS1[(base)+5], lane); \
+    g_ry_d<6>(re0, im0, re1, im1, GC0[(base)+6], GS0[(base)+6], GC1[(base)+6], GS1[(base)+6], lane); \
+    g_ry_d<7>(re0, im0, re1, im1, GC0[(base)+7], GS0[(base)+7], GC1[(base)+7], GS1[(base)+7], lane); \
+    g_ry_d<8>(re0, im0, re1, im1, GC0[(base)+8], GS0[(base)+8], GC1[(base)+8], GS1[(base)+8], lane); \
+    g_ry_d<9>(re0, im0, re1, im1, GC0[(base)+9], GS0[(base)+9], GC1[(base)+9], GS1[(base)+9], lane);
+
+    RING_D(0, false)
+    CD_D(10)
+    RING_D(20, true)
+#define UB_D(i) g_u1_d<i>(re0, im0, re1, im1, &ub[wv][0][(i) * 8], &ub[wv][1][(i) * 8], lane);
+    ALLQ(UB_D)
+#undef UB_D
+    RING_D(30, false)
+    CD_D(40)
+    RING_D(50, true)
+#undef RING_D
+#undef CD_D
+
+    float o0, o1;
+    meas_fold_d(re0, im0, re1, im1, uu[wv], lane, o0, o1);
+    o0 = wred(o0, lane);
+    o1 = wred(o1, lane);
+    if (lane == 0) {
+        if (b0 < B) ws[b0] = o0;
+        if (b1i < B) ws[b1i] = o1;
+    }
 }
 
 __global__ void k_out(const float* __restrict__ ws, float* __restrict__ out, int B) {
@@ -657,9 +718,9 @@
     float* ws  = (float*)d_ws;
 
     const int B = in_sizes[0] / 256;
-    const int nb = (B + 3) / 4;
-
-    hipLaunchKernelGGL(k_main, dim3(nb), dim3(TPB), 0, stream,
+    const int nb = (B + 7) / 8;
+
+    hipLaunchKernelGGL(k_main, dim3(nb + 1), dim3(TPB), 0, stream,
                        x, W_proj, b_proj, qlcu_base, b_params, c_params, dt_params,
                        gate_base, skip_base, W1, b1, W2, b2, W3, b3, w1, w2, w3,
                        W_out, b_out, ws, B);
```
